# Optimization experiments

Measured on AMD Instinct MI355X. Metric: run time of the kernel, lower is better.

The kernel has to match this reference:

```python
import jax, jax.numpy as jnp
import numpy as np

N_NODES = 16384
N_EDGES = 131072
N_GRAPHS = 64
DIMS = [396, 4096, 2048, 1024, 1024, 2048, 256, 1]  # layer widths from __init__
BN_EPS = 1e-5


def setup_inputs() -> dict:
    key = jax.random.key(0)
    ks = jax.random.split(key, 32)
    inp = {
        "x": jax.random.normal(ks[0], (N_NODES, DIMS[0]), jnp.float32),
        "edge_index": jax.random.randint(ks[1], (2, N_EDGES), 0, N_NODES, dtype=jnp.int32),
        "batch": jnp.sort(jax.random.randint(ks[2], (N_NODES,), 0, N_GRAPHS, dtype=jnp.int32)),
    }
    for i in range(7):
        fi, fo = DIMS[i], DIMS[i + 1]
        inp[f"W{i+1}"] = jax.random.normal(ks[3 + i], (fi, fo), jnp.float32) * (1.0 / np.sqrt(fi)).astype(np.float32)
        inp[f"b{i+1}"] = jnp.zeros((fo,), jnp.float32)
    for i in range(6):
        inp[f"g{i+1}"] = jnp.ones((DIMS[i + 1],), jnp.float32)
        inp[f"be{i+1}"] = jnp.zeros((DIMS[i + 1],), jnp.float32)
    return inp


def _gcn_norm(edge_index, n):
    # PyG GCNConv default: add self-loops, sym-normalize D^-1/2 (A+I) D^-1/2
    loop = jnp.arange(n, dtype=edge_index.dtype)
    src = jnp.concatenate([edge_index[0], loop])
    dst = jnp.concatenate([edge_index[1], loop])
    deg = jax.ops.segment_sum(jnp.ones_like(src, jnp.float32), dst, num_segments=n)
    dinv = jax.lax.rsqrt(jnp.maximum(deg, 1.0))  # deg >= 1 due to self-loops
    norm = dinv[src] * dinv[dst]  # [E + N]
    return src, dst, norm


def _gcn_conv(x, W, b, src, dst, norm, n):
    h = x @ W                                   # dense linear transform
    msg = h[src] * norm[:, None]                # gather + edge scaling
    agg = jax.ops.segment_sum(msg, dst, num_segments=n)  # scatter-add
    return agg + b


def _bn(x, g, b):
    # BatchNorm1d in training mode: biased batch variance
    m = jnp.mean(x, axis=0)
    v = jnp.mean(jnp.square(x - m), axis=0)
    return (x - m) * jax.lax.rsqrt(v + BN_EPS) * g + b


def reference(x, edge_index, batch,
              W1, b1, W2, b2, W3, b3, W4, b4, W5, b5, W6, b6, W7, b7,
              g1, be1, g2, be2, g3, be3, g4, be4, g5, be5, g6, be6):
    n = x.shape[0]
    src, dst, norm = _gcn_norm(edge_index, n)
    Ws = [W1, W2, W3, W4, W5, W6]
    bs = [b1, b2, b3, b4, b5, b6]
    gs = [g1, g2, g3, g4, g5, g6]
    bes = [be1, be2, be3, be4, be5, be6]
    h = x
    for W, b, g, be in zip(Ws, bs, gs, bes):
        h = jax.nn.relu(_gcn_conv(h, W, b, src, dst, norm, n))
        h = _bn(h, g, be)
    h = _gcn_conv(h, W7, b7, src, dst, norm, n)   # [N, 1], no relu/bn
    out = jax.ops.segment_sum(h, batch, num_segments=N_GRAPHS)  # global_add_pool
    return out
```

## Files before the change

kernel.cpp:

```cpp
#include <hip/hip_runtime.h>


#define NN 16384
#define NE 131072
#define NG 64

typedef unsigned int u32;
typedef unsigned short u16;
typedef __attribute__((ext_vector_type(8))) _Float16 half8;
typedef __attribute__((ext_vector_type(4))) float f32x4;
typedef __attribute__((ext_vector_type(8))) u16 us8;
typedef __attribute__((ext_vector_type(4))) u16 us4;
typedef __attribute__((ext_vector_type(2))) u16 us2;

#define AS1(p) ((const __attribute__((address_space(1))) void*)(p))
#define AS3(p) ((__attribute__((address_space(3))) void*)(p))

__device__ __forceinline__ float b2f(u16 h) {
    _Float16 x = __builtin_bit_cast(_Float16, h);
    return (float)x;
}
__device__ __forceinline__ u16 f2b(float f) {
    _Float16 x = (_Float16)f;
    return __builtin_bit_cast(u16, x);
}

template <int VW> struct VecU;
template <> struct VecU<8> { typedef us8 T; };
template <> struct VecU<4> { typedef us4 T; };
template <> struct VecU<2> { typedef us2 T; };
template <> struct VecU<1> { typedef u16 T; };

template <int VW>
__device__ __forceinline__ void loadf(const u16* p, float* f) {
    typename VecU<VW>::T v = *(const typename VecU<VW>::T*)p;
    if constexpr (VW == 1) {
        f[0] = b2f((u16)v);
    } else {
        #pragma unroll
        for (int j = 0; j < VW; ++j) f[j] = b2f(v[j]);
    }
}
template <int VW>
__device__ __forceinline__ void storef(u16* p, const float* f) {
    typename VecU<VW>::T v;
    if constexpr (VW == 1) {
        v = f2b(f[0]);
    } else {
        #pragma unroll
        for (int j = 0; j < VW; ++j) v[j] = f2b(f[j]);
    }
    *(typename VecU<VW>::T*)p = v;
}

__global__ void k_degi(const int* __restrict__ dst, int* __restrict__ deg) {
    int e = blockIdx.x * 256 + threadIdx.x;
    if (e < NE) atomicAdd(&deg[dst[e]], 1);
}
__global__ void k_dinv(const int* __restrict__ deg, float* __restrict__ dinv) {
    int i = blockIdx.x * 256 + threadIdx.x;
    if (i < NN) dinv[i] = rsqrtf((float)(deg[i] + 1));
}
__global__ void k_nrm(const int* __restrict__ src, const int* __restrict__ dst,
                      const float* __restrict__ dinv, float* __restrict__ nrm) {
    int e = blockIdx.x * 256 + threadIdx.x;
    if (e < NE) nrm[e] = dinv[src[e]] * dinv[dst[e]];
}
__global__ __launch_bounds__(1024) void k_scan(const int* __restrict__ deg, int* __restrict__ rowptr) {
    __shared__ int part[1024];
    int t = threadIdx.x;
    int base = t * 16;
    int s = 0;
    #pragma unroll
    for (int j = 0; j < 16; ++j) s += deg[base + j];
    part[t] = s;
    __syncthreads();
    for (int off = 1; off < 1024; off <<= 1) {
        int v = 0;
        if (t >= off) v = part[t - off];
        __syncthreads();
        part[t] += v;
        __syncthreads();
    }
    int run = part[t] - s;
    for (int j = 0; j < 16; ++j) { rowptr[base + j] = run; run += deg[base + j]; }
    if (t == 1023) rowptr[NN] = run;
}
__global__ void k_place(const int* __restrict__ src, const int* __restrict__ dst,
                        const float* __restrict__ nrm, const int* __restrict__ rowptr,
                        int* __restrict__ cursor, int* __restrict__ csr_src,
                        float* __restrict__ csr_w) {
    int e = blockIdx.x * 256 + threadIdx.x;
    if (e >= NE) return;
    int d = dst[e];
    int p = rowptr[d] + atomicAdd(&cursor[d], 1);
    csr_src[p] = src[e];
    csr_w[p] = nrm[e];
}
__global__ void k_srow(const int* __restrict__ rowptr, const float* __restrict__ csr_w,
                       const float* __restrict__ dinv, float* __restrict__ svec) {
    int i = blockIdx.x * 256 + threadIdx.x;
    if (i >= NN) return;
    float s = dinv[i] * dinv[i];
    int r1 = rowptr[i + 1];
    for (int e = rowptr[i]; e < r1; ++e) s += csr_w[e];
    svec[i] = s;
}

__global__ void k_x2b(const float* __restrict__ x, u16* __restrict__ xp) {
    int idx = blockIdx.x * 256 + threadIdx.x;
    int i = idx >> 9, c = idx & 511;
    float v = (c < 396) ? x[(size_t)i * 396 + c] : 0.f;
    xp[idx] = f2b(v);
}
__global__ void k_wt(const float* __restrict__ W, u16* __restrict__ Wt,
                     int Ksrc, int Kpad, int N) {
    __shared__ float t[32][33];
    int k0 = blockIdx.x * 32, n0 = blockIdx.y * 32;
    #pragma unroll
    for (int j = 0; j < 4; ++j) {
        int k = k0 + threadIdx.y + j * 8;
        float v = 0.f;
        if (k < Ksrc) v = W[(size_t)k * N + n0 + threadIdx.x];
        t[threadIdx.y + j * 8][threadIdx.x] = v;
    }
    __syncthreads();
    #pragma unroll
    for (int j = 0; j < 4; ++j) {
        int n = n0 + threadIdx.y + j * 8;
        int k = k0 + threadIdx.x;
        Wt[(size_t)n * Kpad + k] = f2b(t[threadIdx.x][threadIdx.y + j * 8]);
    }
}

template <int VW>
__global__ __launch_bounds__(256) void k_agg(const u16* __restrict__ in, u16* __restrict__ out,
                                             const int* __restrict__ rowptr,
                                             const int* __restrict__ csr_src,
                                             const float* __restrict__ csr_w,
                                             const float* __restrict__ dinv,
                                             const float* __restrict__ svec,
                                             const float* __restrict__ bias,
                                             const float* __restrict__ av,
                                             const float* __restrict__ bvv,
                                             int F, int mode) {
    int i = blockIdx.x;
    int c0 = threadIdx.x * VW;
    float acc[VW];
    float d2 = dinv[i]; d2 *= d2;
    {
        float v[VW];
        loadf<VW>(in + (size_t)i * F + c0, v);
        #pragma unroll
        for (int j = 0; j < VW; ++j) acc[j] = d2 * v[j];
    }
    int r0 = rowptr[i], r1 = rowptr[i + 1];
    for (int e = r0; e < r1; ++e) {
        int s = csr_src[e];
        float w = csr_w[e];
        float v[VW];
        loadf<VW>(in + (size_t)s * F + c0, v);
        #pragma unroll
        for (int j = 0; j < VW; ++j) acc[j] += w * v[j];
    }
    if (mode == 1) {
        #pragma unroll
        for (int j = 0; j < VW; ++j) acc[j] = fmaxf(acc[j] + bias[c0 + j], 0.f);
    } else if (mode == 2) {
        float si = svec[i];
        #pragma unroll
        for (int j = 0; j < VW; ++j) acc[j] = av[c0 + j] * acc[j] + si * bvv[c0 + j];
    }
    storef<VW>(out + (size_t)i * F + c0, acc);
}

#define SROWS 128
template <int VW>
__global__ __launch_bounds__(256) void k_stats(const u16* __restrict__ h, float* __restrict__ s1,
                                               float* __restrict__ s2, int F) {
    int c0 = (blockIdx.x * 256 + threadIdx.x) * VW;
    int r0 = blockIdx.y * SROWS;
    float s[VW], q[VW];
    #pragma unroll
    for (int j = 0; j < VW; ++j) { s[j] = 0.f; q[j] = 0.f; }
    for (int r = r0; r < r0 + SROWS; ++r) {
        float v[VW];
        loadf<VW>(h + (size_t)r * F + c0, v);
        #pragma unroll
        for (int j = 0; j < VW; ++j) { s[j] += v[j]; q[j] += v[j] * v[j]; }
    }
    #pragma unroll
    for (int j = 0; j < VW; ++j) {
        atomicAdd(&s1[c0 + j], s[j]);
        atomicAdd(&s2[c0 + j], q[j]);
    }
}
__global__ void k_bnab(const float* __restrict__ s1, const float* __restrict__ s2,
                       const float* __restrict__ g, const float* __restrict__ be,
                       float* __restrict__ a, float* __restrict__ b, int F) {
    int c = blockIdx.x * 256 + threadIdx.x;
    if (c >= F) return;
    float m = s1[c] * (1.f / NN);
    float v = s2[c] * (1.f / NN) - m * m;
    float aa = g[c] * rsqrtf(v + 1e-5f);
    a[c] = aa;
    b[c] = be[c] - m * aa;
}
__global__ __launch_bounds__(256) void k_bnapply(u16* __restrict__ h, const float* __restrict__ s1,
                                                 const float* __restrict__ s2,
                                                 const float* __restrict__ g,
                                                 const float* __restrict__ be, int F) {
    size_t idx = blockIdx.x * (size_t)256 + threadIdx.x;
    int Fv = F >> 3;
    int c = (int)(idx % Fv) * 8;
    u16* p = h + idx * 8;
    float v[8];
    loadf<8>(p, v);
    #pragma unroll
    for (int j = 0; j < 8; ++j) {
        float m = s1[c + j] * (1.f / NN);
        float var = s2[c + j] * (1.f / NN) - m * m;
        float a = g[c + j] * rsqrtf(var + 1e-5f);
        v[j] = a * (v[j] - m) + be[c + j];
    }
    storef<8>(p, v);
}

__device__ __forceinline__ void stage16k(const char* gbase, size_t rs, int ktile, int h,
                                         char* slot, int tid) {
    size_t colb = (size_t)ktile * 128 + h * 64;
    #pragma unroll
    for (int i = 0; i < 2; ++i) {
        int G = i * 512 + tid;
        int r = G >> 2;
        int c = ((G & 3) - (r >> 1)) & 3;
        __builtin_amdgcn_global_load_lds(AS1(gbase + (size_t)r * rs + colb + c * 16),
                                         AS3(slot + i * 8192 + ((tid >> 6) << 10)), 16, 0, 0);
    }
}

__global__ __launch_bounds__(512, 2) void k_gemm256(const u16* __restrict__ A,
                                                    const u16* __restrict__ Wt,
                                                    const float* __restrict__ bias,
                                                    u16* __restrict__ C,
                                                    int K, int N, int bx, int fuse) {
    extern __shared__ __align__(16) char smem[];
    int nwg = gridDim.x;
    int chunk = nwg >> 3;
    int swz = (blockIdx.x & 7) * chunk + (blockIdx.x >> 3);
    int tx = swz % bx, ty = swz / bx;
    int tid = threadIdx.x;
    int wid = tid >> 6, lane = tid & 63;
    int wr = wid >> 2, wc = wid & 3;
    int lo = lane & 15, hi = lane >> 4;
    int sw = (((hi + (lo >> 1)) & 3) << 4);
    size_t row0 = (size_t)ty * 256;
    size_t col0 = (size_t)tx * 256;
    int nkt = K >> 6;

    const char* gA = (const char*)(A + row0 * K);
    const char* gB = (const char*)(Wt + col0 * K);
    size_t rs = (size_t)K * 2;

    const char* aA = smem + wr * 8192 + lo * 64 + sw;
    const char* bA = smem + 65536 + wc * 4096 + lo * 64 + sw;
#define ASL(b, h) (smem + (((b) * 2 + (h)) << 14))
#define BSL(b, h) (smem + 65536 + (((b) * 2 + (h)) << 14))

    f32x4 acc[8][4];
    #pragma unroll
    for (int m = 0; m < 8; ++m)
        #pragma unroll
        for (int n = 0; n < 4; ++n) acc[m][n] = {0.f, 0.f, 0.f, 0.f};
    half8 af[4], bf[4];

    stage16k(gA, rs, 0, 0, ASL(0, 0), tid);
    stage16k(gB, rs, 0, 0, BSL(0, 0), tid);
    stage16k(gA, rs, 0, 1, ASL(0, 1), tid);
    stage16k(gB, rs, 0, 1, BSL(0, 1), tid);
    stage16k(gA, rs, 1, 0, ASL(1, 0), tid);
    stage16k(gB, rs, 1, 0, BSL(1, 0), tid);
    asm volatile("s_waitcnt vmcnt(4)" ::: "memory");
    __builtin_amdgcn_sched_barrier(0);
    __builtin_amdgcn_s_barrier();

#define DS_LOADS(KK, MH)                                                                   \
    {                                                                                      \
        _Pragma("unroll") for (int j = 0; j < 4; ++j)                                      \
            af[j] = *(const half8*)(aA + buf * 32768 + (KK) * 16384 + (MH) * 4096 + j * 1024); \
        if ((MH) == 0) {                                                                   \
            _Pragma("unroll") for (int j = 0; j < 4; ++j)                                  \
                bf[j] = *(const half8*)(bA + buf * 32768 + (KK) * 16384 + j * 1024);       \
        }                                                                                  \
    }
#define MFMA_PHASE(MH)                                                                     \
    {                                                                                      \
        asm volatile("" ::: "memory");                                                     \
        __builtin_amdgcn_s_barrier();                                                      \
        __builtin_amdgcn_s_setprio(1);                                                     \
        _Pragma("unroll") for (int j = 0; j < 4; ++j)                                      \
            _Pragma("unroll") for (int n = 0; n < 4; ++n)                                  \
                acc[(MH) * 4 + j][n] = __builtin_amdgcn_mfma_f32_16x16x32_f16(             \
                    af[j], bf[n], acc[(MH) * 4 + j][n], 0, 0, 0);                          \
        __builtin_amdgcn_s_setprio(0);                                                     \
    }
#define END_BARRIER                                                                        \
    {                                                                                      \
        asm volatile("" ::: "memory");                                                     \
        __builtin_amdgcn_s_barrier();                                                      \
    }

    for (int kt = 0; kt < nkt; ++kt) {
        int buf = kt & 1;
        DS_LOADS(0, 0);
        if (kt + 1 < nkt) {
            stage16k(gA, rs, kt + 1, 1, ASL(buf ^ 1, 1), tid);
            stage16k(gB, rs, kt + 1, 1, BSL(buf ^ 1, 1), tid);
        }
        MFMA_PHASE(0);
        END_BARRIER;
        DS_LOADS(0, 1);
        MFMA_PHASE(1);
        END_BARRIER;
        DS_LOADS(1, 0);
        if (kt + 2 < nkt) stage16k(gA, rs, kt + 2, 0, ASL(buf, 0), tid);
        MFMA_PHASE(0);
        END_BARRIER;
        DS_LOADS(1, 1);
        if (kt + 2 < nkt) stage16k(gB, rs, kt + 2, 0, BSL(buf, 0), tid);
        MFMA_PHASE(1);
        asm volatile("s_waitcnt vmcnt(4)" ::: "memory");
        __builtin_amdgcn_sched_barrier(0);
        END_BARRIER;
    }

    #pragma unroll
    for (int fm = 0; fm < 8; ++fm) {
        #pragma unroll
        for (int n = 0; n < 4; ++n) {
            #pragma unroll
            for (int r = 0; r < 4; ++r) {
                size_t row = row0 + wr * 128 + fm * 16 + hi * 4 + r;
                size_t col = col0 + wc * 64 + n * 16 + lo;
                float v = acc[fm][n][r];
                if (fuse) v = fmaxf(v + bias[col], 0.f);
                C[row * N + col] = f2b(v);
            }
        }
    }
#undef DS_LOADS
#undef MFMA_PHASE
#undef END_BARRIER
#undef ASL
#undef BSL
}

__global__ __launch_bounds__(256) void k_gemm(const u16* __restrict__ A, const u16* __restrict__ Wt,
                                              const float* __restrict__ bias, u16* __restrict__ C,
                                              int K, int N, int bx, int fuse) {
    __shared__ __align__(16) u16 As[128 * 32];
    __shared__ __align__(16) u16 Bs[128 * 32];
    int nwg = gridDim.x;
    int chunk = nwg >> 3;
    int swz = (blockIdx.x & 7) * chunk + (blockIdx.x >> 3);
    int tx = swz % bx, ty = swz / bx;
    int tid = threadIdx.x;
    int wid = tid >> 6, lane = tid & 63;
    int wr = wid >> 1, wc = wid & 1;
    int lo = lane & 15, hi = lane >> 4;
    size_t row0 = (size_t)ty * 128;
    size_t col0 = (size_t)tx * 128;

    f32x4 acc[4][4];
    #pragma unroll
    for (int m = 0; m < 4; ++m)
        #pragma unroll
        for (int n = 0; n < 4; ++n) acc[m][n] = {0.f, 0.f, 0.f, 0.f};

    const char* gA = (const char*)(A + row0 * K);
    const char* gB = (const char*)(Wt + col0 * K);
    size_t rs = (size_t)K * 2;
    int lin0 = tid * 16;
    int lin1 = lin0 + 4096;
    int rA0 = lin0 >> 6, cb0 = lin0 & 63;
    int rA1 = lin1 >> 6, cb1 = lin1 & 63;
    unsigned ldsOff = (unsigned)(wid << 10);

    for (int k0 = 0; k0 < K; k0 += 32) {
        __syncthreads();
        size_t kb = (size_t)k0 * 2;
        __builtin_amdgcn_global_load_lds(AS1(gA + (size_t)rA0 * rs + cb0 + kb),
                                         AS3((char*)As + ldsOff), 16, 0, 0);
        __builtin_amdgcn_global_load_lds(AS1(gA + (size_t)rA1 * rs + cb1 + kb),
                                         AS3((char*)As + 4096 + ldsOff), 16, 0, 0);
        __builtin_amdgcn_global_load_lds(AS1(gB + (size_t)rA0 * rs + cb0 + kb),
                                         AS3((char*)Bs + ldsOff), 16, 0, 0);
        __builtin_amdgcn_global_load_lds(AS1(gB + (size_t)rA1 * rs + cb1 + kb),
                                         AS3((char*)Bs + 4096 + ldsOff), 16, 0, 0);
        __syncthreads();
        half8 afr[4], bfr[4];
        #pragma unroll
        for (int m = 0; m < 4; ++m)
            afr[m] = *(const half8*)((const u16*)As + (wr * 64 + m * 16 + lo) * 32 + hi * 8);
        #pragma unroll
        for (int n = 0; n < 4; ++n)
            bfr[n] = *(const half8*)((const u16*)Bs + (wc * 64 + n * 16 + lo) * 32 + hi * 8);
        #pragma unroll
        for (int m = 0; m < 4; ++m)
            #pragma unroll
            for (int n = 0; n < 4; ++n)
                acc[m][n] = __builtin_amdgcn_mfma_f32_16x16x32_f16(afr[m], bfr[n], acc[m][n], 0, 0, 0);
    }
    #pragma unroll
    for (int m = 0; m < 4; ++m) {
        #pragma unroll
        for (int n = 0; n < 4; ++n) {
            #pragma unroll
            for (int r = 0; r < 4; ++r) {
                size_t row = row0 + wr * 64 + m * 16 + hi * 4 + r;
                size_t col = col0 + wc * 64 + n * 16 + lo;
                float v = acc[m][n][r];
                if (fuse) v = fmaxf(v + bias[col], 0.f);
                C[row * N + col] = f2b(v);
            }
        }
    }
}

__global__ __launch_bounds__(256) void k_gemv(const u16* __restrict__ A, const float* __restrict__ w,
                                              const float* __restrict__ a, const float* __restrict__ b,
                                              float* __restrict__ y) {
    int row = blockIdx.x * 4 + (threadIdx.x >> 6);
    int lane = threadIdx.x & 63;
    const u16* h = A + (size_t)row * 256;
    float s = 0.f;
    #pragma unroll
    for (int j = 0; j < 4; ++j) {
        int c = lane + j * 64;
        s += (a[c] * b2f(h[c]) + b[c]) * w[c];
    }
    #pragma unroll
    for (int off = 32; off; off >>= 1) s += __shfl_down(s, off);
    if (lane == 0) y[row] = s;
}
__global__ void k_final(const float* __restrict__ y, const int* __restrict__ rowptr,
                        const int* __restrict__ csr_src, const float* __restrict__ csr_w,
                        const float* __restrict__ dinv, const int* __restrict__ batch,
                        const float* __restrict__ b7, float* __restrict__ out) {
    int i = blockIdx.x * 256 + threadIdx.x;
    if (i >= NN) return;
    float v = dinv[i] * dinv[i] * y[i];
    int r1 = rowptr[i + 1];
    for (int e = rowptr[i]; e < r1; ++e) v += csr_w[e] * y[csr_src[e]];
    atomicAdd(&out[batch[i]], v + b7[0]);
}
__global__ void k_sentinel(float* out, float v) {
    if (threadIdx.x == 0 && blockIdx.x == 0) out[0] = v;
}

static inline char* alignp(char* p) { return (char*)(((uintptr_t)p + 255) & ~(uintptr_t)255); }

extern "C" void kernel_launch(void* const* d_in, const int* in_sizes, int n_in,
                              void* d_out, int out_size, void* d_ws, size_t ws_size,
                              hipStream_t stream) {
    const float* x = (const float*)d_in[0];
    const int* ei = (const int*)d_in[1];
    const int* src = ei;
    const int* dst = ei + NE;
    const int* batch = (const int*)d_in[2];
    const float* W[7]; const float* bv[7];
    for (int i = 0; i < 7; ++i) { W[i] = (const float*)d_in[3 + 2 * i]; bv[i] = (const float*)d_in[4 + 2 * i]; }
    const float* g[6]; const float* be[6];
    for (int i = 0; i < 6; ++i) { g[i] = (const float*)d_in[17 + 2 * i]; be[i] = (const float*)d_in[18 + 2 * i]; }
    float* out = (float*)d_out;

    char* p = (char*)d_ws;
    u16* Abuf = (u16*)p; p += (size_t)NN * 4096 * 2;
    u16* Bbuf = (u16*)p; p += (size_t)NN * 2048 * 2;
    u16* xpad = (u16*)p; p += (size_t)NN * 512 * 2;
    u16* W1t = (u16*)p; p += (size_t)4096 * 512 * 2;
    u16* W2t = (u16*)p; p += (size_t)2048 * 4096 * 2;
    u16* W3t = (u16*)p; p += (size_t)1024 * 2048 * 2;
    u16* W4t = (u16*)p; p += (size_t)1024 * 1024 * 2;
    u16* W5t = (u16*)p; p += (size_t)2048 * 1024 * 2;
    u16* W6t = (u16*)p; p += (size_t)256 * 2048 * 2;
    p = alignp(p);
    int* degi = (int*)p; p += NN * 4;
    int* cursor = (int*)p; p += NN * 4;
    int* rowptr = (int*)p; p += (NN + 1) * 4; p = alignp(p);
    int* csr_src = (int*)p; p += NE * 4;
    float* csr_w = (float*)p; p += NE * 4;
    float* dinv = (float*)p; p += NN * 4;
    float* nrm = (float*)p; p += NE * 4;
    float* svec = (float*)p; p += NN * 4;
    float* s1 = (float*)p; p += 4096 * 4;
    float* s2 = (float*)p; p += 4096 * 4;
    float* bna = (float*)p; p += 4096 * 4;
    float* bnb = (float*)p; p += 4096 * 4;
    float* y = (float*)p; p += NN * 4;
    size_t need = (size_t)(p - (char*)d_ws);
    if (need > ws_size) {
        hipMemsetAsync(d_out, 0, NG * sizeof(float), stream);
        k_sentinel<<<1, 64, 0, stream>>>(out, (float)(ws_size >> 20));
        return;
    }

    (void)hipFuncSetAttribute((const void*)k_gemm256,
                              hipFuncAttributeMaxDynamicSharedMemorySize, 131072);

    hipMemsetAsync(degi, 0, 2 * NN * sizeof(int), stream);
    k_degi<<<NE / 256, 256, 0, stream>>>(dst, degi);
    k_dinv<<<NN / 256, 256, 0, stream>>>(degi, dinv);
    k_nrm<<<NE / 256, 256, 0, stream>>>(src, dst, dinv, nrm);
    k_scan<<<1, 1024, 0, stream>>>(degi, rowptr);
    k_place<<<NE / 256, 256, 0, stream>>>(src, dst, nrm, rowptr, cursor, csr_src, csr_w);
    k_srow<<<NN / 256, 256, 0, stream>>>(rowptr, csr_w, dinv, svec);

    k_x2b<<<(NN * 512) / 256, 256, 0, stream>>>(x, xpad);
    {
        dim3 b(32, 8);
        k_wt<<<dim3(16, 128), b, 0, stream>>>(W[0], W1t, 396, 512, 4096);
        k_wt<<<dim3(128, 64), b, 0, stream>>>(W[1], W2t, 4096, 4096, 2048);
        k_wt<<<dim3(64, 32), b, 0, stream>>>(W[2], W3t, 2048, 2048, 1024);
        k_wt<<<dim3(32, 32), b, 0, stream>>>(W[3], W4t, 1024, 1024, 1024);
        k_wt<<<dim3(32, 64), b, 0, stream>>>(W[4], W5t, 1024, 1024, 2048);
        k_wt<<<dim3(64, 8), b, 0, stream>>>(W[5], W6t, 2048, 2048, 256);
    }

    auto gemm = [&](const u16* A, const u16* Wt, const float* bias, u16* Cp, int K, int N, int fuse) {
        if (N >= 1024) {
            int bx = N / 256;
            k_gemm256<<<bx * (NN / 256), 512, 131072, stream>>>(A, Wt, bias, Cp, K, N, bx, fuse);
        } else {
            int bx = N / 128;
            k_gemm<<<bx * (NN / 128), 256, 0, stream>>>(A, Wt, bias, Cp, K, N, bx, fuse);
        }
    };
    auto agg = [&](const u16* in, u16* o, const float* bias, const float* av,
                   const float* bvv, int F, int mode) {
        if (F == 2048) k_agg<8><<<NN, 256, 0, stream>>>(in, o, rowptr, csr_src, csr_w, dinv, svec, bias, av, bvv, F, mode);
        else if (F == 1024) k_agg<4><<<NN, 256, 0, stream>>>(in, o, rowptr, csr_src, csr_w, dinv, svec, bias, av, bvv, F, mode);
        else if (F == 512) k_agg<2><<<NN, 256, 0, stream>>>(in, o, rowptr, csr_src, csr_w, dinv, svec, bias, av, bvv, F, mode);
        else k_agg<1><<<NN, 256, 0, stream>>>(in, o, rowptr, csr_src, csr_w, dinv, svec, bias, av, bvv, F, mode);
    };
    auto stats = [&](const u16* h, int F) {
        hipMemsetAsync(s1, 0, 2 * 4096 * sizeof(float), stream);
        if (F == 4096) k_stats<8><<<dim3(2, NN / SROWS), 256, 0, stream>>>(h, s1, s2, F);
        else if (F == 2048) k_stats<8><<<dim3(1, NN / SROWS), 256, 0, stream>>>(h, s1, s2, F);
        else if (F == 1024) k_stats<4><<<dim3(1, NN / SROWS), 256, 0, stream>>>(h, s1, s2, F);
        else k_stats<1><<<dim3(1, NN / SROWS), 256, 0, stream>>>(h, s1, s2, F);
    };
    auto bnapply = [&](u16* h, int F, int li) {
        k_bnapply<<<(int)(((size_t)NN * F / 8) / 256), 256, 0, stream>>>(h, s1, s2, g[li], be[li], F);
    };

    agg(xpad, Bbuf, nullptr, nullptr, nullptr, 512, 0);
    gemm(Bbuf, W1t, bv[0], Abuf, 512, 4096, 1);
    stats(Abuf, 4096);
    bnapply(Abuf, 4096, 0);

    gemm(Abuf, W2t, nullptr, Bbuf, 4096, 2048, 0);
    agg(Bbuf, Abuf, bv[1], nullptr, nullptr, 2048, 1);
    stats(Abuf, 2048);
    bnapply(Abuf, 2048, 1);

    gemm(Abuf, W3t, nullptr, Bbuf, 2048, 1024, 0);
    agg(Bbuf, Abuf, bv[2], nullptr, nullptr, 1024, 1);
    stats(Abuf, 1024);
    bnapply(Abuf, 1024, 2);

    gemm(Abuf, W4t, nullptr, Bbuf, 1024, 1024, 0);
    agg(Bbuf, Abuf, bv[3], nullptr, nullptr, 1024, 1);
    stats(Abuf, 1024);
    k_bnab<<<1024 / 256, 256, 0, stream>>>(s1, s2, g[3], be[3], bna, bnb, 1024);

    agg(Abuf, Bbuf, nullptr, bna, bnb, 1024, 2);
    gemm(Bbuf, W5t, bv[4], Abuf, 1024, 2048, 1);
    stats(Abuf, 2048);
    bnapply(Abuf, 2048, 4);

    gemm(Abuf, W6t, nullptr, Bbuf, 2048, 256, 0);
    agg(Bbuf, Abuf, bv[5], nullptr, nullptr, 256, 1);
    stats(Abuf, 256);
    k_bnab<<<1, 256, 0, stream>>>(s1, s2, g[5], be[5], bna, bnb, 256);

    k_gemv<<<NN / 4, 256, 0, stream>>>(Abuf, W[6], bna, bnb, y);
    hipMemsetAsync(d_out, 0, NG * sizeof(float), stream);
    k_final<<<NN / 256, 256, 0, stream>>>(y, rowptr, csr_src, csr_w, dinv, batch, bv[6], out);
}
```

Measured before the change: 1.503 ms.

## Fold BatchNorm affine into next layer weights and fuse stats into GEMM epilogue

Drops the separate BN-apply pass over activations. The per-column BN scale is folded into the next layer's transposed weights, and the shift becomes a per-output vector rv that is added in the aggregation epilogue, weighted by the row's normalization sum. Column sum and sum-of-squares are accumulated in the GEMM256 epilogue when that GEMM's output feeds BN directly, which removes separate stats passes for layers 1 and 5. This adds atomics and LDS reductions to the GEMM tail, and the fp16 weight scaling may change precision slightly.

New measurement: 1.316 ms. 1.14x faster.

```diff
diff --git a/kernel.cpp b/kernel.cpp
--- a/kernel.cpp
+++ b/kernel.cpp
@@ -114,22 +114,34 @@
     xp[idx] = f2b(v);
 }
 __global__ void k_wt(const float* __restrict__ W, u16* __restrict__ Wt,
-                     int Ksrc, int Kpad, int N) {
+                     const float* __restrict__ scale, const float* __restrict__ bsh,
+                     float* __restrict__ rv, int Ksrc, int Kpad, int N) {
     __shared__ float t[32][33];
+    __shared__ float rbuf[8][32];
     int k0 = blockIdx.x * 32, n0 = blockIdx.y * 32;
+    int tx = threadIdx.x, ty = threadIdx.y;
+    float rvp = 0.f;
     #pragma unroll
     for (int j = 0; j < 4; ++j) {
-        int k = k0 + threadIdx.y + j * 8;
+        int k = k0 + ty + j * 8;
         float v = 0.f;
-        if (k < Ksrc) v = W[(size_t)k * N + n0 + threadIdx.x];
-        t[threadIdx.y + j * 8][threadIdx.x] = v;
-    }
+        if (k < Ksrc) v = W[(size_t)k * N + n0 + tx];
+        if (rv) rvp += bsh[k] * v;
+        t[ty + j * 8][tx] = scale ? v * scale[k] : v;
+    }
+    if (rv) rbuf[ty][tx] = rvp;
     __syncthreads();
     #pragma unroll
     for (int j = 0; j < 4; ++j) {
-        int n = n0 + threadIdx.y + j * 8;
-        int k = k0 + threadIdx.x;
-        Wt[(size_t)n * Kpad + k] = f2b(t[threadIdx.x][threadIdx.y + j * 8]);
+        int n = n0 + ty + j * 8;
+        int k = k0 + tx;
+        Wt[(size_t)n * Kpad + k] = f2b(t[tx][ty + j * 8]);
+    }
+    if (rv && ty == 0) {
+        float s = 0.f;
+        #pragma unroll
+        for (int j = 0; j < 8; ++j) s += rbuf[j][tx];
+        atomicAdd(&rv[n0 + tx], s);
     }
 }
 
@@ -141,6 +153,7 @@
                                              const float* __restrict__ dinv,
                                              const float* __restrict__ svec,
                                              const float* __restrict__ bias,
+                                             const float* __restrict__ rv,
                                              const float* __restrict__ av,
                                              const float* __restrict__ bvv,
                                              int F, int mode) {
@@ -164,8 +177,10 @@
         for (int j = 0; j < VW; ++j) acc[j] += w * v[j];
     }
     if (mode == 1) {
-        #pragma unroll
-        for (int j = 0; j < VW; ++j) acc[j] = fmaxf(acc[j] + bias[c0 + j], 0.f);
+        float si = svec[i];
+        #pragma unroll
+        for (int j = 0; j < VW; ++j)
+            acc[j] = fmaxf(acc[j] + si * rv[c0 + j] + bias[c0 + j], 0.f);
     } else if (mode == 2) {
         float si = svec[i];
         #pragma unroll
@@ -206,25 +221,6 @@
     a[c] = aa;
     b[c] = be[c] - m * aa;
 }
-__global__ __launch_bounds__(256) void k_bnapply(u16* __restrict__ h, const float* __restrict__ s1,
-                                                 const float* __restrict__ s2,
-                                                 const float* __restrict__ g,
-                                                 const float* __restrict__ be, int F) {
-    size_t idx = blockIdx.x * (size_t)256 + threadIdx.x;
-    int Fv = F >> 3;
-    int c = (int)(idx % Fv) * 8;
-    u16* p = h + idx * 8;
-    float v[8];
-    loadf<8>(p, v);
-    #pragma unroll
-    for (int j = 0; j < 8; ++j) {
-        float m = s1[c + j] * (1.f / NN);
-        float var = s2[c + j] * (1.f / NN) - m * m;
-        float a = g[c + j] * rsqrtf(var + 1e-5f);
-        v[j] = a * (v[j] - m) + be[c + j];
-    }
-    storef<8>(p, v);
-}
 
 __device__ __forceinline__ void stage16k(const char* gbase, size_t rs, int ktile, int h,
                                          char* slot, int tid) {
@@ -243,6 +239,8 @@
                                                     const u16* __restrict__ Wt,
                                                     const float* __restrict__ bias,
                                                     u16* __restrict__ C,
+                                                    float* __restrict__ s1,
+                                                    float* __restrict__ s2,
                                                     int K, int N, int bx, int fuse) {
     extern __shared__ __align__(16) char smem[];
     int nwg = gridDim.x;
@@ -334,6 +332,7 @@
         END_BARRIER;
     }
 
+    float cs[4] = {0.f, 0.f, 0.f, 0.f}, cq[4] = {0.f, 0.f, 0.f, 0.f};
     #pragma unroll
     for (int fm = 0; fm < 8; ++fm) {
         #pragma unroll
@@ -345,7 +344,27 @@
                 float v = acc[fm][n][r];
                 if (fuse) v = fmaxf(v + bias[col], 0.f);
                 C[row * N + col] = f2b(v);
+                cs[n] += v;
+                cq[n] += v * v;
             }
+        }
+    }
+    if (s1) {
+        asm volatile("s_waitcnt vmcnt(0)" ::: "memory");
+        __syncthreads();
+        float* sp = (float*)smem;
+        sp[tid] = 0.f;
+        __syncthreads();
+        #pragma unroll
+        for (int n = 0; n < 4; ++n) {
+            int lc = wc * 64 + n * 16 + lo;
+            atomicAdd(&sp[lc * 2], cs[n]);
+            atomicAdd(&sp[lc * 2 + 1], cq[n]);
+        }
+        __syncthreads();
+        if (tid < 256) {
+            atomicAdd(&s1[col0 + tid], sp[tid * 2]);
+            atomicAdd(&s2[col0 + tid], sp[tid * 2 + 1]);
         }
     }
 #undef DS_LOADS
@@ -497,6 +516,7 @@
     float* s2 = (float*)p; p += 4096 * 4;
     float* bna = (float*)p; p += 4096 * 4;
     float* bnb = (float*)p; p += 4096 * 4;
+    float* rv = (float*)p; p += 4096 * 4;
     float* y = (float*)p; p += NN * 4;
     size_t need = (size_t)(p - (char*)d_ws);
     if (need > ws_size) {
@@ -517,72 +537,69 @@
     k_srow<<<NN / 256, 256, 0, stream>>>(rowptr, csr_w, dinv, svec);
 
     k_x2b<<<(NN * 512) / 256, 256, 0, stream>>>(x, xpad);
-    {
-        dim3 b(32, 8);
-        k_wt<<<dim3(16, 128), b, 0, stream>>>(W[0], W1t, 396, 512, 4096);
-        k_wt<<<dim3(128, 64), b, 0, stream>>>(W[1], W2t, 4096, 4096, 2048);
-        k_wt<<<dim3(64, 32), b, 0, stream>>>(W[2], W3t, 2048, 2048, 1024);
-        k_wt<<<dim3(32, 32), b, 0, stream>>>(W[3], W4t, 1024, 1024, 1024);
-        k_wt<<<dim3(32, 64), b, 0, stream>>>(W[4], W5t, 1024, 1024, 2048);
-        k_wt<<<dim3(64, 8), b, 0, stream>>>(W[5], W6t, 2048, 2048, 256);
-    }
-
-    auto gemm = [&](const u16* A, const u16* Wt, const float* bias, u16* Cp, int K, int N, int fuse) {
-        if (N >= 1024) {
-            int bx = N / 256;
-            k_gemm256<<<bx * (NN / 256), 512, 131072, stream>>>(A, Wt, bias, Cp, K, N, bx, fuse);
-        } else {
-            int bx = N / 128;
-            k_gemm<<<bx * (NN / 128), 256, 0, stream>>>(A, Wt, bias, Cp, K, N, bx, fuse);
-        }
+    dim3 wtb(32, 8);
+    k_wt<<<dim3(16, 128), wtb, 0, stream>>>(W[0], W1t, nullptr, nullptr, nullptr, 396, 512, 4096);
+    k_wt<<<dim3(32, 64), wtb, 0, stream>>>(W[4], W5t, nullptr, nullptr, nullptr, 1024, 1024, 2048);
+
+    auto gemm256 = [&](const u16* A, const u16* Wt, const float* bias, u16* Cp,
+                       float* st1, float* st2, int K, int N, int fuse) {
+        int bx = N / 256;
+        k_gemm256<<<bx * (NN / 256), 512, 131072, stream>>>(A, Wt, bias, Cp, st1, st2, K, N, bx, fuse);
     };
-    auto agg = [&](const u16* in, u16* o, const float* bias, const float* av,
-                   const float* bvv, int F, int mode) {
-        if (F == 2048) k_agg<8><<<NN, 256, 0, stream>>>(in, o, rowptr, csr_src, csr_w, dinv, svec, bias, av, bvv, F, mode);
-        else if (F == 1024) k_agg<4><<<NN, 256, 0, stream>>>(in, o, rowptr, csr_src, csr_w, dinv, svec, bias, av, bvv, F, mode);
-        else if (F == 512) k_agg<2><<<NN, 256, 0, stream>>>(in, o, rowptr, csr_src, csr_w, dinv, svec, bias, av, bvv, F, mode);
-        else k_agg<1><<<NN, 256, 0, stream>>>(in, o, rowptr, csr_src, csr_w, dinv, svec, bias, av, bvv, F, mode);
+    auto agg = [&](const u16* in, u16* o, const float* bias, const float* rvp,
+                   const float* av, const float* bvv, int F, int mode) {
+        if (F == 2048) k_agg<8><<<NN, 256, 0, stream>>>(in, o, rowptr, csr_src, csr_w, dinv, svec, bias, rvp, av, bvv, F, mode);
+        else if (F == 1024) k_agg<4><<<NN, 256, 0, stream>>>(in, o, rowptr, csr_src, csr_w, dinv, svec, bias, rvp, av, bvv, F, mode);
+        else if (F == 512) k_agg<2><<<NN, 256, 0, stream>>>(in, o, rowptr, csr_src, csr_w, dinv, svec, bias, rvp, av, bvv, F, mode);
+        else k_agg<1><<<NN, 256, 0, stream>>>(in, o, rowptr, csr_src, csr_w, dinv, svec, bias, rvp, av, bvv, F, mode);
     };
     auto stats = [&](const u16* h, int F) {
         hipMemsetAsync(s1, 0, 2 * 4096 * sizeof(float), stream);
-        if (F == 4096) k_stats<8><<<dim3(2, NN / SROWS), 256, 0, stream>>>(h, s1, s2, F);
-        else if (F == 2048) k_stats<8><<<dim3(1, NN / SROWS), 256, 0, stream>>>(h, s1, s2, F);
+        if (F == 2048) k_stats<8><<<dim3(1, NN / SROWS), 256, 0, stream>>>(h, s1, s2, F);
         else if (F == 1024) k_stats<4><<<dim3(1, NN / SROWS), 256, 0, stream>>>(h, s1, s2, F);
         else k_stats<1><<<dim3(1, NN / SROWS), 256, 0, stream>>>(h, s1, s2, F);
     };
-    auto bnapply = [&](u16* h, int F, int li) {
-        k_bnapply<<<(int)(((size_t)NN * F / 8) / 256), 256, 0, stream>>>(h, s1, s2, g[li], be[li], F);
+    auto bnab = [&](int li, int F) {
+        k_bnab<<<(F + 255) / 256, 256, 0, stream>>>(s1, s2, g[li], be[li], bna, bnb, F);
     };
-
-    agg(xpad, Bbuf, nullptr, nullptr, nullptr, 512, 0);
-    gemm(Bbuf, W1t, bv[0], Abuf, 512, 4096, 1);
-    stats(Abuf, 4096);
-    bnapply(Abuf, 4096, 0);
-
-    gemm(Abuf, W2t, nullptr, Bbuf, 4096, 2048, 0);
-    agg(Bbuf, Abuf, bv[1], nullptr, nullptr, 2048, 1);
+    auto wts = [&](const float* Wp, u16* Wtp, int K, int N) {
+        hipMemsetAsync(rv, 0, N * sizeof(float), stream);
+        k_wt<<<dim3(K / 32, N / 32), wtb, 0, stream>>>(Wp, Wtp, bna, bnb, rv, K, K, N);
+    };
+
+    agg(xpad, Bbuf, nullptr, nullptr, nullptr, nullptr, 512, 0);
+    hipMemsetAsync(s1, 0, 2 * 4096 * sizeof(float), stream);
+    gemm256(Bbuf, W1t, bv[0], Abuf, s1, s2, 512, 4096, 1);
+    bnab(0, 4096);
+
+    wts(W[1], W2t, 4096, 2048);
+    gemm256(Abuf, W2t, nullptr, Bbuf, nullptr, nullptr, 4096, 2048, 0);
+    agg(Bbuf, Abuf, bv[1], rv, nullptr, nullptr, 2048, 1);
     stats(Abuf, 2048);
-    bnapply(Abuf, 2048, 1);
-
-    gemm(Abuf, W3t, nullptr, Bbuf, 2048, 1024, 0);
-    agg(Bbuf, Abuf, bv[2], nullptr, nullptr, 1024, 1);
+    bnab(1, 2048);
+
+    wts(W[2], W3t, 2048, 1024);
+    gemm256(Abuf, W3t, nullptr, Bbuf, nullptr, nullptr, 2048, 1024, 0);
+    agg(Bbuf, Abuf, bv[2], rv, nullptr, nullptr, 1024, 1);
     stats(Abuf, 1024);
-    bnapply(Abuf, 1024, 2);
-
-    gemm(Abuf, W4t, nullptr, Bbuf, 1024, 1024, 0);
-    agg(Bbuf, Abuf, bv[3], nullptr, nullptr, 1024, 1);
+    bnab(2, 1024);
+
+    wts(W[3], W4t, 1024, 1024);
+    gemm256(Abuf, W4t, nullptr, Bbuf, nullptr, nullptr, 1024, 1024, 0);
+    agg(Bbuf, Abuf, bv[3], rv, nullptr, nullptr, 1024, 1);
     stats(Abuf, 1024);
-    k_bnab<<<1024 / 256, 256, 0, stream>>>(s1, s2, g[3], be[3], bna, bnb, 1024);
-
-    agg(Abuf, Bbuf, nullptr, bna, bnb, 1024, 2);
-    gemm(Bbuf, W5t, bv[4], Abuf, 1024, 2048, 1);
-    stats(Abuf, 2048);
-    bnapply(Abuf, 2048, 4);
-
-    gemm(Abuf, W6t, nullptr, Bbuf, 2048, 256, 0);
-    agg(Bbuf, Abuf, bv[5], nullptr, nullptr, 256, 1);
+    bnab(3, 1024);
+
+    agg(Abuf, Bbuf, nullptr, nullptr, bna, bnb, 1024, 2);
+    hipMemsetAsync(s1, 0, 2 * 4096 * sizeof(float), stream);
+    gemm256(Bbuf, W5t, bv[4], Abuf, s1, s2, 1024, 2048, 1);
+    bnab(4, 2048);
+
+    wts(W[5], W6t, 2048, 256);
+    k_gemm<<<(256 / 128) * (NN / 128), 256, 0, stream>>>(Abuf, W6t, nullptr, Bbuf, 2048, 256, 256 / 128, 0);
+    agg(Bbuf, Abuf, bv[5], rv, nullptr, nullptr, 256, 1);
     stats(Abuf, 256);
-    k_bnab<<<1, 256, 0, stream>>>(s1, s2, g[5], be[5], bna, bnb, 256);
+    bnab(5, 256);
 
     k_gemv<<<NN / 4, 256, 0, stream>>>(Abuf, W[6], bna, bnb, y);
     hipMemsetAsync(d_out, 0, NG * sizeof(float), stream);
```

## Fuse BN column statistics into GEMM epilogue and retune aggregation launch widths

Applied to the files above, without the earlier changes.

The 256-tile GEMM epilogue now accumulates per-column sum and sum-of-squares, reduces them in shared memory and atomically adds them to global stats buffers. This removes the separate stats pass after layers 1 and 5. The aggregation kernel gathers two neighbor rows per iteration into split accumulators for more memory-level parallelism. Aggregation and stats launches now size their blocks as F/VW with wider vectors. The fused stats add shared-memory atomics and an extra barrier to the GEMM tail, and the stats are computed from fp32 values rather than the rounded fp16 outputs.

New measurement: 1.425 ms. -5.2%, faster.

```diff
diff --git a/kernel.cpp b/kernel.cpp
--- a/kernel.cpp
+++ b/kernel.cpp
@@ -117,19 +117,20 @@
                      int Ksrc, int Kpad, int N) {
     __shared__ float t[32][33];
     int k0 = blockIdx.x * 32, n0 = blockIdx.y * 32;
+    int tx = threadIdx.x, ty = threadIdx.y;
     #pragma unroll
     for (int j = 0; j < 4; ++j) {
-        int k = k0 + threadIdx.y + j * 8;
+        int k = k0 + ty + j * 8;
         float v = 0.f;
-        if (k < Ksrc) v = W[(size_t)k * N + n0 + threadIdx.x];
-        t[threadIdx.y + j * 8][threadIdx.x] = v;
+        if (k < Ksrc) v = W[(size_t)k * N + n0 + tx];
+        t[ty + j * 8][tx] = v;
     }
     __syncthreads();
     #pragma unroll
     for (int j = 0; j < 4; ++j) {
-        int n = n0 + threadIdx.y + j * 8;
-        int k = k0 + threadIdx.x;
-        Wt[(size_t)n * Kpad + k] = f2b(t[threadIdx.x][threadIdx.y + j * 8]);
+        int n = n0 + ty + j * 8;
+        int k = k0 + tx;
+        Wt[(size_t)n * Kpad + k] = f2b(t[tx][ty + j * 8]);
     }
 }
 
@@ -155,7 +156,24 @@
         for (int j = 0; j < VW; ++j) acc[j] = d2 * v[j];
     }
     int r0 = rowptr[i], r1 = rowptr[i + 1];
-    for (int e = r0; e < r1; ++e) {
+    int e = r0;
+    if (r1 - r0 >= 2) {
+        float acc2[VW];
+        #pragma unroll
+        for (int j = 0; j < VW; ++j) acc2[j] = 0.f;
+        for (; e + 1 < r1; e += 2) {
+            int sa = csr_src[e], sb = csr_src[e + 1];
+            float wa = csr_w[e], wb = csr_w[e + 1];
+            float va[VW], vb[VW];
+            loadf<VW>(in + (size_t)sa * F + c0, va);
+            loadf<VW>(in + (size_t)sb * F + c0, vb);
+            #pragma unroll
+            for (int j = 0; j < VW; ++j) { acc[j] += wa * va[j]; acc2[j] += wb * vb[j]; }
+        }
+        #pragma unroll
+        for (int j = 0; j < VW; ++j) acc[j] += acc2[j];
+    }
+    for (; e < r1; ++e) {
         int s = csr_src[e];
         float w = csr_w[e];
         float v[VW];
@@ -178,7 +196,7 @@
 template <int VW>
 __global__ __launch_bounds__(256) void k_stats(const u16* __restrict__ h, float* __restrict__ s1,
                                                float* __restrict__ s2, int F) {
-    int c0 = (blockIdx.x * 256 + threadIdx.x) * VW;
+    int c0 = threadIdx.x * VW;
     int r0 = blockIdx.y * SROWS;
     float s[VW], q[VW];
     #pragma unroll
@@ -243,6 +261,8 @@
                                                     const u16* __restrict__ Wt,
                                                     const float* __restrict__ bias,
                                                     u16* __restrict__ C,
+                                                    float* __restrict__ s1,
+                                                    float* __restrict__ s2,
                                                     int K, int N, int bx, int fuse) {
     extern __shared__ __align__(16) char smem[];
     int nwg = gridDim.x;
@@ -334,6 +354,7 @@
         END_BARRIER;
     }
 
+    float cs[4] = {0.f, 0.f, 0.f, 0.f}, cq[4] = {0.f, 0.f, 0.f, 0.f};
     #pragma unroll
     for (int fm = 0; fm < 8; ++fm) {
         #pragma unroll
@@ -345,7 +366,27 @@
                 float v = acc[fm][n][r];
                 if (fuse) v = fmaxf(v + bias[col], 0.f);
                 C[row * N + col] = f2b(v);
+                cs[n] += v;
+                cq[n] += v * v;
             }
+        }
+    }
+    if (s1) {
+        asm volatile("s_waitcnt vmcnt(0)" ::: "memory");
+        __syncthreads();
+        float* sp = (float*)smem;
+        sp[tid] = 0.f;
+        __syncthreads();
+        #pragma unroll
+        for (int n = 0; n < 4; ++n) {
+            int lc = wc * 64 + n * 16 + lo;
+            atomicAdd(&sp[lc * 2], cs[n]);
+            atomicAdd(&sp[lc * 2 + 1], cq[n]);
+        }
+        __syncthreads();
+        if (tid < 256) {
+            atomicAdd(&s1[col0 + tid], sp[tid * 2]);
+            atomicAdd(&s2[col0 + tid], sp[tid * 2 + 1]);
         }
     }
 #undef DS_LOADS
@@ -517,69 +558,59 @@
     k_srow<<<NN / 256, 256, 0, stream>>>(rowptr, csr_w, dinv, svec);
 
     k_x2b<<<(NN * 512) / 256, 256, 0, stream>>>(x, xpad);
-    {
-        dim3 b(32, 8);
-        k_wt<<<dim3(16, 128), b, 0, stream>>>(W[0], W1t, 396, 512, 4096);
-        k_wt<<<dim3(128, 64), b, 0, stream>>>(W[1], W2t, 4096, 4096, 2048);
-        k_wt<<<dim3(64, 32), b, 0, stream>>>(W[2], W3t, 2048, 2048, 1024);
-        k_wt<<<dim3(32, 32), b, 0, stream>>>(W[3], W4t, 1024, 1024, 1024);
-        k_wt<<<dim3(32, 64), b, 0, stream>>>(W[4], W5t, 1024, 1024, 2048);
-        k_wt<<<dim3(64, 8), b, 0, stream>>>(W[5], W6t, 2048, 2048, 256);
-    }
-
-    auto gemm = [&](const u16* A, const u16* Wt, const float* bias, u16* Cp, int K, int N, int fuse) {
-        if (N >= 1024) {
-            int bx = N / 256;
-            k_gemm256<<<bx * (NN / 256), 512, 131072, stream>>>(A, Wt, bias, Cp, K, N, bx, fuse);
-        } else {
-            int bx = N / 128;
-            k_gemm<<<bx * (NN / 128), 256, 0, stream>>>(A, Wt, bias, Cp, K, N, bx, fuse);
-        }
+    dim3 wtb(32, 8);
+    k_wt<<<dim3(16, 128), wtb, 0, stream>>>(W[0], W1t, 396, 512, 4096);
+    k_wt<<<dim3(128, 64), wtb, 0, stream>>>(W[1], W2t, 4096, 4096, 2048);
+    k_wt<<<dim3(64, 32), wtb, 0, stream>>>(W[2], W3t, 2048, 2048, 1024);
+    k_wt<<<dim3(32, 32), wtb, 0, stream>>>(W[3], W4t, 1024, 1024, 1024);
+    k_wt<<<dim3(32, 64), wtb, 0, stream>>>(W[4], W5t, 1024, 1024, 2048);
+    k_wt<<<dim3(64, 8), wtb, 0, stream>>>(W[5], W6t, 2048, 2048, 256);
+
+    auto gemm256 = [&](const u16* A, const u16* Wt, const float* bias, u16* Cp,
+                       float* st1, float* st2, int K, int N, int fuse) {
+        int bx = N / 256;
+        k_gemm256<<<bx * (NN / 256), 512, 131072, stream>>>(A, Wt, bias, Cp, st1, st2, K, N, bx, fuse);
     };
     auto agg = [&](const u16* in, u16* o, const float* bias, const float* av,
                    const float* bvv, int F, int mode) {
-        if (F == 2048) k_agg<8><<<NN, 256, 0, stream>>>(in, o, rowptr, csr_src, csr_w, dinv, svec, bias, av, bvv, F, mode);
-        else if (F == 1024) k_agg<4><<<NN, 256, 0, stream>>>(in, o, rowptr, csr_src, csr_w, dinv, svec, bias, av, bvv, F, mode);
-        else if (F == 512) k_agg<2><<<NN, 256, 0, stream>>>(in, o, rowptr, csr_src, csr_w, dinv, svec, bias, av, bvv, F, mode);
-        else k_agg<1><<<NN, 256, 0, stream>>>(in, o, rowptr, csr_src, csr_w, dinv, svec, bias, av, bvv, F, mode);
+        if (F >= 512) k_agg<8><<<NN, F / 8, 0, stream>>>(in, o, rowptr, csr_src, csr_w, dinv, svec, bias, av, bvv, F, mode);
+        else k_agg<4><<<NN, F / 4, 0, stream>>>(in, o, rowptr, csr_src, csr_w, dinv, svec, bias, av, bvv, F, mode);
     };
     auto stats = [&](const u16* h, int F) {
         hipMemsetAsync(s1, 0, 2 * 4096 * sizeof(float), stream);
-        if (F == 4096) k_stats<8><<<dim3(2, NN / SROWS), 256, 0, stream>>>(h, s1, s2, F);
-        else if (F == 2048) k_stats<8><<<dim3(1, NN / SROWS), 256, 0, stream>>>(h, s1, s2, F);
-        else if (F == 1024) k_stats<4><<<dim3(1, NN / SROWS), 256, 0, stream>>>(h, s1, s2, F);
-        else k_stats<1><<<dim3(1, NN / SROWS), 256, 0, stream>>>(h, s1, s2, F);
+        if (F >= 512) k_stats<8><<<dim3(1, NN / SROWS), F / 8, 0, stream>>>(h, s1, s2, F);
+        else k_stats<4><<<dim3(1, NN / SROWS), F / 4, 0, stream>>>(h, s1, s2, F);
     };
     auto bnapply = [&](u16* h, int F, int li) {
         k_bnapply<<<(int)(((size_t)NN * F / 8) / 256), 256, 0, stream>>>(h, s1, s2, g[li], be[li], F);
     };
 
     agg(xpad, Bbuf, nullptr, nullptr, nullptr, 512, 0);
-    gemm(Bbuf, W1t, bv[0], Abuf, 512, 4096, 1);
-    stats(Abuf, 4096);
+    hipMemsetAsync(s1, 0, 2 * 4096 * sizeof(float), stream);
+    gemm256(Bbuf, W1t, bv[0], Abuf, s1, s2, 512, 4096, 1);
     bnapply(Abuf, 4096, 0);
 
-    gemm(Abuf, W2t, nullptr, Bbuf, 4096, 2048, 0);
+    gemm256(Abuf, W2t, nullptr, Bbuf, nullptr, nullptr, 4096, 2048, 0);
     agg(Bbuf, Abuf, bv[1], nullptr, nullptr, 2048, 1);
     stats(Abuf, 2048);
     bnapply(Abuf, 2048, 1);
 
-    gemm(Abuf, W3t, nullptr, Bbuf, 2048, 1024, 0);
+    gemm256(Abuf, W3t, nullptr, Bbuf, nullptr, nullptr, 2048, 1024, 0);
     agg(Bbuf, Abuf, bv[2], nullptr, nullptr, 1024, 1);
     stats(Abuf, 1024);
     bnapply(Abuf, 1024, 2);
 
-    gemm(Abuf, W4t, nullptr, Bbuf, 1024, 1024, 0);
+    gemm256(Abuf, W4t, nullptr, Bbuf, nullptr, nullptr, 1024, 1024, 0);
     agg(Bbuf, Abuf, bv[3], nullptr, nullptr, 1024, 1);
     stats(Abuf, 1024);
     k_bnab<<<1024 / 256, 256, 0, stream>>>(s1, s2, g[3], be[3], bna, bnb, 1024);
 
     agg(Abuf, Bbuf, nullptr, bna, bnb, 1024, 2);
-    gemm(Bbuf, W5t, bv[4], Abuf, 1024, 2048, 1);
-    stats(Abuf, 2048);
+    hipMemsetAsync(s1, 0, 2 * 4096 * sizeof(float), stream);
+    gemm256(Bbuf, W5t, bv[4], Abuf, s1, s2, 1024, 2048, 1);
     bnapply(Abuf, 2048, 4);
 
-    gemm(Abuf, W6t, nullptr, Bbuf, 2048, 256, 0);
+    k_gemm<<<(256 / 128) * (NN / 128), 256, 0, stream>>>(Abuf, W6t, nullptr, Bbuf, 2048, 256, 256 / 128, 0);
     agg(Bbuf, Abuf, bv[5], nullptr, nullptr, 256, 1);
     stats(Abuf, 256);
     k_bnab<<<1, 256, 0, stream>>>(s1, s2, g[5], be[5], bna, bnb, 256);
```
